# Kernel tuning notes

Hardware: AMD Instinct MI355X
Metric: run time of the kernel (lower is better)

Reference implementation:

```python
import jax, jax.numpy as jnp
import numpy as np

M = 12          # input channels / groups
OUT_DIM = 48    # qkv conv out channels (multiple of M)
HIDDEN = 768    # hidden_size; LN over HIDDEN // M = 64
KSIZE = 3
B, S, N = 8, 1024, HIDDEN // M
LN_EPS = 1e-5


def _gconv(x, w, b, groups):
    # x: [B, Cin, S, N]; w: [Cout, Cin//groups, k, k] (OIHW); stride 1, SAME pad == (k-1)//2
    y = jax.lax.conv_general_dilated(
        x, w, window_strides=(1, 1), padding='SAME',
        dimension_numbers=('NCHW', 'OIHW', 'NCHW'),
        feature_group_count=groups)
    return y + b[None, :, None, None]


def setup_inputs() -> dict:
    key = jax.random.key(0)
    ks = jax.random.split(key, 10)
    s_qkv = 1.0 / np.sqrt(KSIZE * KSIZE)           # fan_in = 1 * k * k (groups=m)
    s_1 = 1.0 / np.sqrt(OUT_DIM)                    # fan_in = out_dim * 1 * 1
    return {
        'x':  jax.random.normal(ks[0], (B, M, S, N), dtype=jnp.float32),
        'wq': jax.random.normal(ks[1], (OUT_DIM, 1, KSIZE, KSIZE), dtype=jnp.float32) * s_qkv,
        'bq': jax.random.normal(ks[2], (OUT_DIM,), dtype=jnp.float32) * s_qkv,
        'wk': jax.random.normal(ks[3], (OUT_DIM, 1, KSIZE, KSIZE), dtype=jnp.float32) * s_qkv,
        'bk': jax.random.normal(ks[4], (OUT_DIM,), dtype=jnp.float32) * s_qkv,
        'wv': jax.random.normal(ks[5], (OUT_DIM, 1, KSIZE, KSIZE), dtype=jnp.float32) * s_qkv,
        'bv': jax.random.normal(ks[6], (OUT_DIM,), dtype=jnp.float32) * s_qkv,
        'w1': jax.random.normal(ks[7], (M, OUT_DIM), dtype=jnp.float32) * s_1,  # 1x1 conv squeezed
        'b1': jax.random.normal(ks[8], (M,), dtype=jnp.float32) * s_1,
        'ln_w': jnp.ones((N,), dtype=jnp.float32),
        'ln_b': jnp.zeros((N,), dtype=jnp.float32),
    }


def reference(x, wq, bq, wk, bk, wv, bv, w1, b1, ln_w, ln_b):
    gelu = lambda t: jax.nn.gelu(t, approximate=False)  # torch nn.GELU default (erf)
    # grouped-conv projections + GELU (dropout rate 0 -> identity)
    q = gelu(_gconv(x, wq, bq, M))  # [B, OUT_DIM, S, N]
    k = gelu(_gconv(x, wk, bk, M))
    v = gelu(_gconv(x, wv, bv, M))
    # reshape to [B, S, OUT_DIM*N] (q, v) and [B, OUT_DIM*N, S] (k)
    q2 = jnp.transpose(q, (0, 2, 1, 3)).reshape(B, S, OUT_DIM * N)
    k2 = jnp.transpose(k, (0, 1, 3, 2)).reshape(B, OUT_DIM * N, S)
    v2 = jnp.transpose(v, (0, 2, 1, 3)).reshape(B, S, OUT_DIM * N)
    score = jnp.einsum('bsd,bdt->bst', q2, k2) / jnp.sqrt(jnp.float32(HIDDEN))
    score = jax.nn.softmax(score, axis=-1)
    o = jnp.einsum('bst,btd->bsd', score, v2)           # [B, S, OUT_DIM*N]
    o = jnp.transpose(o.reshape(B, S, OUT_DIM, N), (0, 2, 1, 3))  # [B, OUT_DIM, S, N]
    # 1x1 conv OUT_DIM -> M
    o = jnp.einsum('bosn,mo->bmsn', o, w1) + b1[None, :, None, None]
    # LayerNorm over last dim (N = hidden_size // m)
    mu = jnp.mean(o, axis=-1, keepdims=True)
    var = jnp.mean(jnp.square(o - mu), axis=-1, keepdims=True)
    o = (o - mu) * jax.lax.rsqrt(var + LN_EPS) * ln_w + ln_b
    return o + x
```

## Files before the change

### kernel.cpp

```cpp
#include <hip/hip_runtime.h>

typedef __attribute__((ext_vector_type(8))) short short8;
typedef __attribute__((ext_vector_type(4))) float f32x4;

__device__ __forceinline__ unsigned short f2bf(float f) {
  unsigned u = __float_as_uint(f);
  u += 0x7fffu + ((u >> 16) & 1u);
  return (unsigned short)(u >> 16);
}
__device__ __forceinline__ float bf2f(unsigned short h) {
  return __uint_as_float(((unsigned)h) << 16);
}
__device__ __forceinline__ unsigned pk_bf16(float lo, float hi) {
  unsigned r;
  asm("v_cvt_pk_bf16_f32 %0, %1, %2" : "=v"(r) : "v"(lo), "v"(hi));
  return r;
}
__device__ __forceinline__ float gelu_f(float v) {
  const float t = v * v;
  const float w = fmaf(0.0356774081f, t, 0.7978845608f);
  const float u = v * w;
  const float e = __expf(u + u);
  const float d = e + 1.0f;
  const float r = __builtin_amdgcn_rcpf(d);
  const float th = fmaf(-2.0f, r, 1.0f);
  const float h = 0.5f * v;
  return fmaf(h, th, h);
}
__device__ __forceinline__ void gload16(const void* g, void* l) {
  __builtin_amdgcn_global_load_lds((const __attribute__((address_space(1))) void*)g,
                                   (__attribute__((address_space(3))) void*)l, 16, 0, 0);
}

__global__ __launch_bounds__(256) void conv_qkv_kernel(
    const float* __restrict__ x,
    const float* __restrict__ wq, const float* __restrict__ bq,
    const float* __restrict__ wk, const float* __restrict__ bk,
    const float* __restrict__ wv, const float* __restrict__ bv,
    unsigned short* __restrict__ qb, unsigned short* __restrict__ kb,
    unsigned short* __restrict__ vtb) {
  __shared__ float sin_[66][68];
  const int tid = threadIdx.x;
  const int b = blockIdx.z, g = blockIdx.y;
  const int s0 = blockIdx.x << 6;
  const float* xp = x + ((size_t)(b * 12 + g) << 16);
  for (int i = tid; i < 66 * 64; i += 256) {
    const int r = i >> 6, n = i & 63;
    const int s = s0 - 1 + r;
    sin_[r][n + 1] = (s >= 0 && s < 1024) ? xp[(s << 6) + n] : 0.0f;
  }
  if (tid < 66) { sin_[tid][0] = 0.0f; sin_[tid][65] = 0.0f; sin_[tid][66] = 0.0f; sin_[tid][67] = 0.0f; }
  __syncthreads();

  {
    const int n0 = (tid & 15) << 2;
    const int rb = (tid >> 4) << 2;
    float W[8][9], Bi[8];
#pragma unroll
    for (int j = 0; j < 4; ++j) {
      const int oc = (g << 2) + j;
#pragma unroll
      for (int t = 0; t < 9; ++t) { W[j][t] = wq[oc * 9 + t]; W[4 + j][t] = wk[oc * 9 + t]; }
      Bi[j] = bq[oc]; Bi[4 + j] = bk[oc];
    }
    float rA[6], rB[6], rC[6];
#define LDROW(dst, ridx)                                                              \
    { const float4 p0 = *reinterpret_cast<const float4*>(&sin_[ridx][n0]);            \
      const float2 p1 = *reinterpret_cast<const float2*>(&sin_[ridx][n0 + 4]);        \
      dst[0] = p0.x; dst[1] = p0.y; dst[2] = p0.z; dst[3] = p0.w;                     \
      dst[4] = p1.x; dst[5] = p1.y; }
    LDROW(rA, rb)
    LDROW(rB, rb + 1)
#pragma unroll
    for (int i = 0; i < 4; ++i) {
      const int s = rb + i;
      LDROW(rC, s + 2)
      float pa[8][4];
#pragma unroll
      for (int j = 0; j < 8; ++j)
#pragma unroll
        for (int q = 0; q < 4; ++q) {
          float a = Bi[j];
#pragma unroll
          for (int dc = 0; dc < 3; ++dc) {
            a = fmaf(W[j][dc], rA[q + dc], a);
            a = fmaf(W[j][3 + dc], rB[q + dc], a);
            a = fmaf(W[j][6 + dc], rC[q + dc], a);
          }
          pa[j][q] = a;
        }
#pragma unroll
      for (int j = 0; j < 8; ++j)
#pragma unroll
        for (int q = 0; q < 4; ++q) pa[j][q] = gelu_f(pa[j][q]);
#pragma unroll
      for (int j = 0; j < 8; ++j) {
        const int oc = (g << 2) + (j & 3);
        unsigned short* dst = (j < 4) ? qb : kb;
        uint2 pk;
        pk.x = pk_bf16(pa[j][0], pa[j][1]);
        pk.y = pk_bf16(pa[j][2], pa[j][3]);
        *reinterpret_cast<uint2*>(dst + (((b * 48 + oc) << 16) + ((s0 + s) << 6) + n0)) = pk;
      }
#pragma unroll
      for (int c = 0; c < 6; ++c) { rA[c] = rB[c]; rB[c] = rC[c]; }
    }
#undef LDROW
  }

  {
    const int sp = (tid & 31) << 1;
    const int nb = (tid >> 5) << 3;
    float W[4][9], Bi[4];
#pragma unroll
    for (int j = 0; j < 4; ++j) {
      const int oc = (g << 2) + j;
#pragma unroll
      for (int t = 0; t < 9; ++t) W[j][t] = wv[oc * 9 + t];
      Bi[j] = bv[oc];
    }
    float c0[4], c1[4], c2[4];
#pragma unroll
    for (int r = 0; r < 4; ++r) { c0[r] = sin_[sp + r][nb]; c1[r] = sin_[sp + r][nb + 1]; }
#pragma unroll
    for (int i = 0; i < 8; ++i) {
      const int n = nb + i;
#pragma unroll
      for (int r = 0; r < 4; ++r) c2[r] = sin_[sp + r][n + 2];
      float pa[4][2];
#pragma unroll
      for (int j = 0; j < 4; ++j)
#pragma unroll
        for (int ss = 0; ss < 2; ++ss) {
          float a = Bi[j];
#pragma unroll
          for (int dr = 0; dr < 3; ++dr) {
            a = fmaf(W[j][dr * 3 + 0], c0[ss + dr], a);
            a = fmaf(W[j][dr * 3 + 1], c1[ss + dr], a);
            a = fmaf(W[j][dr * 3 + 2], c2[ss + dr], a);
          }
          pa[j][ss] = a;
        }
#pragma unroll
      for (int j = 0; j < 4; ++j)
#pragma unroll
        for (int ss = 0; ss < 2; ++ss) pa[j][ss] = gelu_f(pa[j][ss]);
#pragma unroll
      for (int j = 0; j < 4; ++j) {
        const size_t d = (size_t)b * 3072 + ((((g << 2) + j) << 6) + n);
        *reinterpret_cast<unsigned*>(vtb + ((d << 10) + s0 + sp)) = pk_bf16(pa[j][0], pa[j][1]);
      }
#pragma unroll
      for (int r = 0; r < 4; ++r) { c0[r] = c1[r]; c1[r] = c2[r]; }
    }
  }
}

__global__ __launch_bounds__(256) void qk_kernel(
    const unsigned short* __restrict__ q, const unsigned short* __restrict__ k,
    float* __restrict__ score) {
  __shared__ __align__(16) unsigned short As[128 * 64];
  __shared__ __align__(16) unsigned short Bs[128 * 64];
  const int tid = threadIdx.x;
  const int w = tid >> 6, lane = tid & 63;
  const int b = blockIdx.z;
  const int s0 = blockIdx.y << 7, t0 = blockIdx.x << 7;
  const int wm = w >> 1, wn = w & 1;
  const int l15 = lane & 15, lhi = lane >> 4;
  f32x4 acc[4][4] = {};

  const unsigned short* qbase = q + ((b * 48) << 16) + (s0 << 6);
  const unsigned short* kbase = k + ((b * 48) << 16) + (t0 << 6);

  for (int c = 0; c < 48; ++c) {
    const unsigned short* qa = qbase + (c << 16);
    const unsigned short* ka = kbase + (c << 16);
    __syncthreads();
#pragma unroll
    for (int i = 0; i < 4; ++i) {
      const int fe = ((i * 4 + w) << 9) + (lane << 3);
      const int lb = (i * 4 + w) << 10;
      gload16(qa + fe, (char*)As + lb);
      gload16(ka + fe, (char*)Bs + lb);
    }
    __syncthreads();
#pragma unroll
    for (int kk = 0; kk < 2; ++kk) {
      const int kc = (kk << 5) + (lhi << 3);
      short8 aF[4], bF[4];
#pragma unroll
      for (int m = 0; m < 4; ++m)
        aF[m] = *reinterpret_cast<const short8*>(&As[((wm << 6) + (m << 4) + l15) * 64 + kc]);
#pragma unroll
      for (int n = 0; n < 4; ++n)
        bF[n] = *reinterpret_cast<const short8*>(&Bs[((wn << 6) + (n << 4) + l15) * 64 + kc]);
#pragma unroll
      for (int m = 0; m < 4; ++m)
#pragma unroll
        for (int n = 0; n < 4; ++n)
          acc[m][n] = __builtin_amdgcn_mfma_f32_16x16x32_bf16(aF[m], bF[n], acc[m][n], 0, 0, 0);
    }
  }
  const float scale = 0.03608439182435161f;
#pragma unroll
  for (int m = 0; m < 4; ++m) {
    const int row = (wm << 6) + (m << 4) + (lhi << 2);
#pragma unroll
    for (int n = 0; n < 4; ++n) {
      const int col = (wn << 6) + (n << 4) + l15;
      float* op = score + ((size_t)((b << 10) + s0 + row) << 10) + t0 + col;
#pragma unroll
      for (int r = 0; r < 4; ++r) op[(size_t)r << 10] = acc[m][n][r] * scale;
    }
  }
}

__global__ __launch_bounds__(256) void softmax_kernel(
    const float* __restrict__ score, unsigned short* __restrict__ p) {
  __shared__ float redm[4], reds[4];
  const int row = blockIdx.x;
  const int tid = threadIdx.x;
  const int w = tid >> 6, lane = tid & 63;
  const float* sr = score + ((size_t)row << 10);
  const float4 v = reinterpret_cast<const float4*>(sr)[tid];
  float mx = fmaxf(fmaxf(v.x, v.y), fmaxf(v.z, v.w));
#pragma unroll
  for (int o = 1; o < 64; o <<= 1) mx = fmaxf(mx, __shfl_xor(mx, o));
  if (lane == 0) redm[w] = mx;
  __syncthreads();
  mx = fmaxf(fmaxf(redm[0], redm[1]), fmaxf(redm[2], redm[3]));
  const float e0 = __expf(v.x - mx), e1 = __expf(v.y - mx);
  const float e2 = __expf(v.z - mx), e3 = __expf(v.w - mx);
  float s = e0 + e1 + e2 + e3;
#pragma unroll
  for (int o = 1; o < 64; o <<= 1) s += __shfl_xor(s, o);
  if (lane == 0) reds[w] = s;
  __syncthreads();
  s = reds[0] + reds[1] + reds[2] + reds[3];
  const float inv = 1.0f / s;
  uint2 pk;
  pk.x = pk_bf16(e0 * inv, e1 * inv);
  pk.y = pk_bf16(e2 * inv, e3 * inv);
  *reinterpret_cast<uint2*>(&p[((size_t)row << 10) + (tid << 2)]) = pk;
}

__global__ __launch_bounds__(256) void pv_kernel(
    const unsigned short* __restrict__ p, const unsigned short* __restrict__ vt,
    unsigned short* __restrict__ o2) {
  __shared__ __align__(16) unsigned short As[128 * 64];
  __shared__ __align__(16) unsigned short Bs[128 * 64];
  const int tid = threadIdx.x;
  const int w = tid >> 6, lane = tid & 63;
  const int b = blockIdx.z;
  const int s0 = blockIdx.y << 7, d0 = blockIdx.x << 7;
  const int wm = w >> 1, wn = w & 1;
  const int l15 = lane & 15, lhi = lane >> 4;
  f32x4 acc[4][4] = {};

  const unsigned short* pbase = p + ((size_t)(b << 10) << 10);
  const unsigned short* vbase = vt + ((size_t)(b * 3072 + d0) << 10);

  for (int t0k = 0; t0k < 1024; t0k += 64) {
    __syncthreads();
#pragma unroll
    for (int i = 0; i < 4; ++i) {
      const int e = (i << 8) + tid;
      const int rr = e >> 3;
      const int cc = (e & 7) << 3;
      const int lb = (i * 4 + w) << 10;
      gload16(pbase + ((size_t)(s0 + rr) << 10) + t0k + cc, (char*)As + lb);
      gload16(vbase + ((size_t)rr << 10) + t0k + cc, (char*)Bs + lb);
    }
    __syncthreads();
#pragma unroll
    for (int kk = 0; kk < 2; ++kk) {
      const int kc = (kk << 5) + (lhi << 3);
      short8 aF[4], bF[4];
#pragma unroll
      for (int m = 0; m < 4; ++m)
        aF[m] = *reinterpret_cast<const short8*>(&As[((wm << 6) + (m << 4) + l15) * 64 + kc]);
#pragma unroll
      for (int n = 0; n < 4; ++n)
        bF[n] = *reinterpret_cast<const short8*>(&Bs[((wn << 6) + (n << 4) + l15) * 64 + kc]);
#pragma unroll
      for (int m = 0; m < 4; ++m)
#pragma unroll
        for (int n = 0; n < 4; ++n)
          acc[m][n] = __builtin_amdgcn_mfma_f32_16x16x32_bf16(aF[m], bF[n], acc[m][n], 0, 0, 0);
    }
  }
#pragma unroll
  for (int m = 0; m < 4; ++m) {
    const int row = (wm << 6) + (m << 4) + (lhi << 2);
#pragma unroll
    for (int n = 0; n < 4; ++n) {
      const int col = (wn << 6) + (n << 4) + l15;
      unsigned short* op = o2 + ((size_t)((b << 10) + s0 + row)) * 3072 + d0 + col;
#pragma unroll
      for (int r = 0; r < 4; ++r) op[(size_t)r * 3072] = f2bf(acc[m][n][r]);
    }
  }
}

__global__ __launch_bounds__(256) void out_kernel(
    const unsigned short* __restrict__ o2, const float* __restrict__ x,
    const float* __restrict__ w1, const float* __restrict__ b1,
    const float* __restrict__ lnw, const float* __restrict__ lnb,
    float* __restrict__ out) {
  const int tid = threadIdx.x;
  const int w = tid >> 6, lane = tid & 63;
  const int row = (blockIdx.x << 2) + w;
  const int b = row >> 10, s = row & 1023;
  const unsigned short* op = o2 + (size_t)row * 3072 + lane;
  float ov[48];
#pragma unroll
  for (int c = 0; c < 48; ++c) ov[c] = bf2f(op[c << 6]);
  float acc[12];
#pragma unroll
  for (int m = 0; m < 12; ++m) {
    float a = b1[m];
#pragma unroll
    for (int c = 0; c < 48; ++c) a = fmaf(ov[c], w1[m * 48 + c], a);
    acc[m] = a;
  }
  const float wn_ = lnw[lane], bn_ = lnb[lane];
#pragma unroll
  for (int m = 0; m < 12; ++m) {
    float s1 = acc[m], s2 = acc[m] * acc[m];
#pragma unroll
    for (int o = 1; o < 64; o <<= 1) { s1 += __shfl_xor(s1, o); s2 += __shfl_xor(s2, o); }
    const float mu = s1 * 0.015625f;
    const float var = s2 * 0.015625f - mu * mu;
    const float rs = rsqrtf(var + 1e-5f);
    const size_t xi = ((size_t)(b * 12 + m) << 16) + (s << 6) + lane;
    out[xi] = (acc[m] - mu) * rs * wn_ + bn_ + x[xi];
  }
}

extern "C" void kernel_launch(void* const* d_in, const int* in_sizes, int n_in,
                              void* d_out, int out_size, void* d_ws, size_t ws_size,
                              hipStream_t stream) {
  (void)in_sizes; (void)n_in; (void)out_size; (void)ws_size;
  const float* x   = (const float*)d_in[0];
  const float* wq  = (const float*)d_in[1];
  const float* bq  = (const float*)d_in[2];
  const float* wk  = (const float*)d_in[3];
  const float* bk  = (const float*)d_in[4];
  const float* wv  = (const float*)d_in[5];
  const float* bv  = (const float*)d_in[6];
  const float* w1  = (const float*)d_in[7];
  const float* b1  = (const float*)d_in[8];
  const float* lnw = (const float*)d_in[9];
  const float* lnb = (const float*)d_in[10];

  char* ws = (char*)d_ws;
  unsigned short* qb  = (unsigned short*)(ws);
  unsigned short* kb  = (unsigned short*)(ws + 50331648);
  unsigned short* vtb = (unsigned short*)(ws + 100663296);
  float*          sc  = (float*)(ws + 150994944);
  unsigned short* pb  = (unsigned short*)(ws + 184549376);
  unsigned short* o2b = (unsigned short*)(ws);
  float* outp = (float*)d_out;

  conv_qkv_kernel<<<dim3(16, 12, 8), 256, 0, stream>>>(x, wq, bq, wk, bk, wv, bv, qb, kb, vtb);
  qk_kernel<<<dim3(8, 8, 8), 256, 0, stream>>>(qb, kb, sc);
  softmax_kernel<<<dim3(8192), 256, 0, stream>>>(sc, pb);
  pv_kernel<<<dim3(24, 8, 8), 256, 0, stream>>>(pb, vtb, o2b);
  out_kernel<<<dim3(2048), 256, 0, stream>>>(o2b, x, w1, b1, lnw, lnb, outp);
}
```

Measured before the change: 241.1 us.

## Double-buffer LDS tiles and XOR-swizzle layout in QK and PV GEMMs

Both GEMM kernels now use two LDS buffers, so the global-to-LDS load for the next K-chunk is issued before computing on the current one, with a vmcnt(0) drain plus barrier between stages. Global-load column blocks are XOR-swizzled by row and the fragment reads apply the matching swizzle, to cut LDS bank conflicts on the short8 reads. This doubles LDS use per block to 64KB, which may reduce occupancy. The full drain at each stage also limits how much load latency is actually hidden.

```diff
diff --git a/kernel.cpp b/kernel.cpp
--- a/kernel.cpp
+++ b/kernel.cpp
@@ -32,6 +32,10 @@
                                    (__attribute__((address_space(3))) void*)l, 16, 0, 0);
 }
 
+#define DRAIN_BAR { asm volatile("s_waitcnt vmcnt(0)" ::: "memory"); \
+                    __builtin_amdgcn_s_barrier();                     \
+                    asm volatile("" ::: "memory"); }
+
 __global__ __launch_bounds__(256) void conv_qkv_kernel(
     const float* __restrict__ x,
     const float* __restrict__ wq, const float* __restrict__ bq,
@@ -156,51 +160,65 @@
   }
 }
 
+#define GEMM_COMPUTE(A_, B_) {                                                          \
+    _Pragma("unroll")                                                                   \
+    for (int kk = 0; kk < 2; ++kk) {                                                    \
+      const int pos = ((((kk << 2) + lhi) ^ (l15 & 7)) << 3);                           \
+      short8 aF[4], bF[4];                                                              \
+      _Pragma("unroll")                                                                 \
+      for (int m = 0; m < 4; ++m)                                                       \
+        aF[m] = *reinterpret_cast<const short8*>(&(A_)[(((wm << 6) + (m << 4) + l15) << 6) + pos]); \
+      _Pragma("unroll")                                                                 \
+      for (int n = 0; n < 4; ++n)                                                       \
+        bF[n] = *reinterpret_cast<const short8*>(&(B_)[(((wn << 6) + (n << 4) + l15) << 6) + pos]); \
+      _Pragma("unroll")                                                                 \
+      for (int m = 0; m < 4; ++m)                                                       \
+        _Pragma("unroll")                                                               \
+        for (int n = 0; n < 4; ++n)                                                     \
+          acc[m][n] = __builtin_amdgcn_mfma_f32_16x16x32_bf16(aF[m], bF[n], acc[m][n], 0, 0, 0); \
+    } }
+
 __global__ __launch_bounds__(256) void qk_kernel(
     const unsigned short* __restrict__ q, const unsigned short* __restrict__ k,
     float* __restrict__ score) {
-  __shared__ __align__(16) unsigned short As[128 * 64];
-  __shared__ __align__(16) unsigned short Bs[128 * 64];
+  __shared__ __align__(16) unsigned short As0[128 * 64], As1[128 * 64];
+  __shared__ __align__(16) unsigned short Bs0[128 * 64], Bs1[128 * 64];
   const int tid = threadIdx.x;
   const int w = tid >> 6, lane = tid & 63;
   const int b = blockIdx.z;
   const int s0 = blockIdx.y << 7, t0 = blockIdx.x << 7;
   const int wm = w >> 1, wn = w & 1;
   const int l15 = lane & 15, lhi = lane >> 4;
+  const int srow = lane >> 3;
+  const int scb = (lane & 7) ^ srow;
   f32x4 acc[4][4] = {};
 
   const unsigned short* qbase = q + ((b * 48) << 16) + (s0 << 6);
   const unsigned short* kbase = k + ((b * 48) << 16) + (t0 << 6);
 
-  for (int c = 0; c < 48; ++c) {
-    const unsigned short* qa = qbase + (c << 16);
-    const unsigned short* ka = kbase + (c << 16);
-    __syncthreads();
-#pragma unroll
-    for (int i = 0; i < 4; ++i) {
-      const int fe = ((i * 4 + w) << 9) + (lane << 3);
-      const int lb = (i * 4 + w) << 10;
-      gload16(qa + fe, (char*)As + lb);
-      gload16(ka + fe, (char*)Bs + lb);
-    }
-    __syncthreads();
-#pragma unroll
-    for (int kk = 0; kk < 2; ++kk) {
-      const int kc = (kk << 5) + (lhi << 3);
-      short8 aF[4], bF[4];
-#pragma unroll
-      for (int m = 0; m < 4; ++m)
-        aF[m] = *reinterpret_cast<const short8*>(&As[((wm << 6) + (m << 4) + l15) * 64 + kc]);
-#pragma unroll
-      for (int n = 0; n < 4; ++n)
-        bF[n] = *reinterpret_cast<const short8*>(&Bs[((wn << 6) + (n << 4) + l15) * 64 + kc]);
-#pragma unroll
-      for (int m = 0; m < 4; ++m)
-#pragma unroll
-        for (int n = 0; n < 4; ++n)
-          acc[m][n] = __builtin_amdgcn_mfma_f32_16x16x32_bf16(aF[m], bF[n], acc[m][n], 0, 0, 0);
-    }
-  }
+#define QK_STAGE(cs, A_, B_) {                                        \
+    const unsigned short* qa = qbase + ((cs) << 16);                  \
+    const unsigned short* ka = kbase + ((cs) << 16);                  \
+    _Pragma("unroll")                                                 \
+    for (int i = 0; i < 4; ++i) {                                     \
+      const int fe = ((((i * 4 + w) << 3) + srow) << 6) + (scb << 3); \
+      const int lb = (i * 4 + w) << 10;                               \
+      gload16(qa + fe, (char*)(A_) + lb);                             \
+      gload16(ka + fe, (char*)(B_) + lb);                             \
+    } }
+
+  QK_STAGE(0, As0, Bs0)
+  DRAIN_BAR
+  for (int c2 = 0; c2 < 24; ++c2) {
+    const int c0 = c2 << 1;
+    QK_STAGE(c0 + 1, As1, Bs1)
+    GEMM_COMPUTE(As0, Bs0)
+    DRAIN_BAR
+    if (c0 + 2 < 48) QK_STAGE(c0 + 2, As0, Bs0)
+    GEMM_COMPUTE(As1, Bs1)
+    DRAIN_BAR
+  }
+#undef QK_STAGE
   const float scale = 0.03608439182435161f;
 #pragma unroll
   for (int m = 0; m < 4; ++m) {
@@ -247,48 +265,43 @@
 __global__ __launch_bounds__(256) void pv_kernel(
     const unsigned short* __restrict__ p, const unsigned short* __restrict__ vt,
     unsigned short* __restrict__ o2) {
-  __shared__ __align__(16) unsigned short As[128 * 64];
-  __shared__ __align__(16) unsigned short Bs[128 * 64];
+  __shared__ __align__(16) unsigned short As0[128 * 64], As1[128 * 64];
+  __shared__ __align__(16) unsigned short Bs0[128 * 64], Bs1[128 * 64];
   const int tid = threadIdx.x;
   const int w = tid >> 6, lane = tid & 63;
   const int b = blockIdx.z;
   const int s0 = blockIdx.y << 7, d0 = blockIdx.x << 7;
   const int wm = w >> 1, wn = w & 1;
   const int l15 = lane & 15, lhi = lane >> 4;
+  const int srow = lane >> 3;
+  const int scb = (lane & 7) ^ srow;
   f32x4 acc[4][4] = {};
 
   const unsigned short* pbase = p + ((size_t)(b << 10) << 10);
   const unsigned short* vbase = vt + ((size_t)(b * 3072 + d0) << 10);
 
-  for (int t0k = 0; t0k < 1024; t0k += 64) {
-    __syncthreads();
-#pragma unroll
-    for (int i = 0; i < 4; ++i) {
-      const int e = (i << 8) + tid;
-      const int rr = e >> 3;
-      const int cc = (e & 7) << 3;
-      const int lb = (i * 4 + w) << 10;
-      gload16(pbase + ((size_t)(s0 + rr) << 10) + t0k + cc, (char*)As + lb);
-      gload16(vbase + ((size_t)rr << 10) + t0k + cc, (char*)Bs + lb);
-    }
-    __syncthreads();
-#pragma unroll
-    for (int kk = 0; kk < 2; ++kk) {
-      const int kc = (kk << 5) + (lhi << 3);
-      short8 aF[4], bF[4];
-#pragma unroll
-      for (int m = 0; m < 4; ++m)
-        aF[m] = *reinterpret_cast<const short8*>(&As[((wm << 6) + (m << 4) + l15) * 64 + kc]);
-#pragma unroll
-      for (int n = 0; n < 4; ++n)
-        bF[n] = *reinterpret_cast<const short8*>(&Bs[((wn << 6) + (n << 4) + l15) * 64 + kc]);
-#pragma unroll
-      for (int m = 0; m < 4; ++m)
-#pragma unroll
-        for (int n = 0; n < 4; ++n)
-          acc[m][n] = __builtin_amdgcn_mfma_f32_16x16x32_bf16(aF[m], bF[n], acc[m][n], 0, 0, 0);
-    }
-  }
+#define PV_STAGE(t0k, A_, B_) {                                          \
+    _Pragma("unroll")                                                    \
+    for (int i = 0; i < 4; ++i) {                                        \
+      const int rr = ((i * 4 + w) << 3) + srow;                          \
+      const int cc = (t0k) + (scb << 3);                                 \
+      const int lb = (i * 4 + w) << 10;                                  \
+      gload16(pbase + ((size_t)(s0 + rr) << 10) + cc, (char*)(A_) + lb); \
+      gload16(vbase + ((size_t)rr << 10) + cc, (char*)(B_) + lb);        \
+    } }
+
+  PV_STAGE(0, As0, Bs0)
+  DRAIN_BAR
+  for (int t2 = 0; t2 < 8; ++t2) {
+    const int t0k = t2 << 7;
+    PV_STAGE(t0k + 64, As1, Bs1)
+    GEMM_COMPUTE(As0, Bs0)
+    DRAIN_BAR
+    if (t0k + 128 < 1024) PV_STAGE(t0k + 128, As0, Bs0)
+    GEMM_COMPUTE(As1, Bs1)
+    DRAIN_BAR
+  }
+#undef PV_STAGE
 #pragma unroll
   for (int m = 0; m < 4; ++m) {
     const int row = (wm << 6) + (m << 4) + (lhi << 2);
```

Measured after the change: 216.9 us. 10.0% less time.
